# Kernel optimization log

Measured on AMD Instinct MI355X. Metric: run time of the kernel, lower is better.

The kernel has to match this reference:

```python
import jax, jax.numpy as jnp
from jax import lax
import numpy as np
import math

DIM = 96      # channels
HEADS = 3     # num_heads
WS = 8        # window size
SHIFT = 4     # window_size // 2 (depth is odd -> shifted)
TLC = 64      # tlc_kernel
H = 264
W = 264


def _grid_idxes(h, w, k1, k2):
    # Faithful replication of the torch grids() tiling index logic (static ints).
    num_row = (h - 1) // k1 + 1
    num_col = (w - 1) // k2 + 1
    step_j = k2 if num_col == 1 else math.ceil((w - k2) / (num_col - 1) - 1e-8)
    step_i = k1 if num_row == 1 else math.ceil((h - k1) / (num_row - 1) - 1e-8)
    idxes = []
    i = 0
    last_i = False
    while i < h and not last_i:
        j = 0
        if i + k1 >= h:
            i = h - k1
            last_i = True
        last_j = False
        while j < w and not last_j:
            if j + k2 >= w:
                j = w - k2
                last_j = True
            idxes.append((i, j))
            j = j + step_j
        i = i + step_i
    return idxes


def setup_inputs() -> dict:
    key = jax.random.key(0)
    ks = jax.random.split(key, 4)
    return {
        "x": jax.random.normal(ks[0], (1, DIM, H, W), jnp.float32),
        "temperature": jnp.ones((HEADS, 1, 1), jnp.float32),
        "qkv_w": jax.random.normal(ks[1], (3 * DIM, DIM), jnp.float32) * 0.05,
        "dw_w": jax.random.normal(ks[2], (3 * DIM, 1, 3, 3), jnp.float32) * 0.1,
        "proj_w": jax.random.normal(ks[3], (DIM, DIM), jnp.float32) * 0.05,
    }


def reference(x, temperature, qkv_w, dw_w, proj_w):
    b, c, h, w = x.shape
    # depth % 2 == 1 -> cyclic shift
    x = jnp.roll(x, (-SHIFT, -SHIFT), axis=(2, 3))
    # 1x1 pointwise conv (no bias)
    qkv = jnp.einsum('oc,bchw->bohw', qkv_w, x)
    # 3x3 depthwise conv, padding 1
    qkv = lax.conv_general_dilated(
        qkv, dw_w, window_strides=(1, 1), padding=[(1, 1), (1, 1)],
        feature_group_count=3 * c, dimension_numbers=('NCHW', 'OIHW', 'NCHW'))
    # --- TLC grids: overlapping tiles (eval path, b == 1) ---
    k1, k2 = min(h, TLC), min(w, TLC)
    idxes = _grid_idxes(h, w, k1, k2)
    parts = jnp.concatenate([qkv[:, :, i:i + k1, j:j + k2] for (i, j) in idxes], axis=0)  # [T,3c,k1,k2]
    T, C3, th, tw = parts.shape
    nh, nw = th // WS, tw // WS
    # window partition: b c (h b0) (w b1) -> (b h w) c b0 b1 -> flatten spatial
    win = parts.reshape(T, C3, nh, WS, nw, WS).transpose(0, 2, 4, 1, 3, 5)
    win = win.reshape(T * nh * nw, C3, WS * WS)  # [Bw, 3c, 64]
    q, k, v = jnp.split(win, 3, axis=1)  # each [Bw, c, 64]
    ch = c // HEADS
    q = q.reshape(-1, HEADS, ch, WS * WS)
    k = k.reshape(-1, HEADS, ch, WS * WS)
    v = v.reshape(-1, HEADS, ch, WS * WS)
    # L2 normalize along token dim (F.normalize eps=1e-12)
    q = q / jnp.maximum(jnp.linalg.norm(q, axis=-1, keepdims=True), 1e-12)
    k = k / jnp.maximum(jnp.linalg.norm(k, axis=-1, keepdims=True), 1e-12)
    # channel attention: [Bw, head, ch, ch]
    attn = jax.nn.relu(jnp.einsum('bhcn,bhdn->bhcd', q, k) * temperature)
    out = jnp.einsum('bhcd,bhdn->bhcn', attn, v)  # [Bw, head, ch, 64]
    out = out.reshape(-1, c, WS, WS)
    # window merge back to tiles
    out = out.reshape(T, nh, nw, c, WS, WS).transpose(0, 3, 1, 4, 2, 5).reshape(T, c, th, tw)
    # --- TLC grids_inverse: scatter-add overlapping tiles and average ---
    preds = jnp.zeros((b, c, h, w), x.dtype)
    cnt = np.zeros((h, w), np.float32)
    for t, (i, j) in enumerate(idxes):
        preds = preds.at[0, :, i:i + k1, j:j + k2].add(out[t])
        cnt[i:i + k1, j:j + k2] += 1.0
    preds = preds / jnp.asarray(cnt)
    # 1x1 output projection
    out = jnp.einsum('oc,bchw->bohw', proj_w, preds)
    # undo cyclic shift
    return jnp.roll(out, (SHIFT, SHIFT), axis=(2, 3))
```

## Files before the change

### kernel.cpp

```cpp
#include <hip/hip_runtime.h>
#include <hip/hip_bf16.h>

#define HW_ 69696
#define W_ 264
#define H_ 264

typedef short bf16x8 __attribute__((ext_vector_type(8)));
typedef float f32x4 __attribute__((ext_vector_type(4)));

static __device__ __forceinline__ unsigned short f2b(float f) {
  __hip_bfloat16 h = __float2bfloat16(f);
  return *reinterpret_cast<unsigned short*>(&h);
}
static __device__ __forceinline__ float b2f(unsigned short u) {
  __hip_bfloat16 h;
  *reinterpret_cast<unsigned short*>(&h) = u;
  return __bfloat162float(h);
}
static __device__ __forceinline__ float lo_f(unsigned int u) {
  union { unsigned int i; float f; } c; c.i = u << 16; return c.f;
}
static __device__ __forceinline__ float hi_f(unsigned int u) {
  union { unsigned int i; float f; } c; c.i = u & 0xffff0000u; return c.f;
}

__global__ __launch_bounds__(256, 5) void k_gemm(const float* __restrict__ x,
                                                 const float* __restrict__ w,
                                                 unsigned short* __restrict__ outb) {
  __shared__ __align__(16) unsigned short As[96 * 104];

  const int tid = threadIdx.x;
  const int wid = tid >> 6, lane = tid & 63;
  const int quad = lane >> 4, lo = lane & 15;
  const int px0 = blockIdx.x * 64;
  const int px = px0 + wid * 16 + lo;

  const int y = px / W_, xx = px - y * W_;
  int y2 = y + 4; if (y2 >= H_) y2 -= H_;
  int x2 = xx + 4; if (x2 >= W_) x2 -= W_;
  const float* xb = x + y2 * W_ + x2;

  bf16x8 bfv[3];
#pragma unroll
  for (int ks = 0; ks < 3; ++ks) {
    const float* xp = xb + (size_t)(ks * 32 + quad * 8) * HW_;
    float f[8];
#pragma unroll
    for (int i = 0; i < 8; ++i) f[i] = xp[(size_t)i * HW_];
    union { bf16x8 v; unsigned short s[8]; } u;
#pragma unroll
    for (int i = 0; i < 8; ++i) u.s[i] = f2b(f[i]);
    bfv[ks] = u.v;
  }

  for (int oc = 0; oc < 3; ++oc) {
    __syncthreads();
    const float* wp = w + oc * 96 * 96;
    for (int l = tid; l < 96 * 24; l += 256) {
      int o = l / 24, c4 = (l - (l / 24) * 24) * 4;
      float4 v = *(const float4*)&wp[o * 96 + c4];
      unsigned int p0 = (unsigned int)f2b(v.x) | ((unsigned int)f2b(v.y) << 16);
      unsigned int p1 = (unsigned int)f2b(v.z) | ((unsigned int)f2b(v.w) << 16);
      *(uint2*)&As[o * 104 + c4] = make_uint2(p0, p1);
    }
    __syncthreads();

    f32x4 acc[6];
#pragma unroll
    for (int mt = 0; mt < 6; ++mt) acc[mt] = {0.f, 0.f, 0.f, 0.f};
#pragma unroll
    for (int ks = 0; ks < 3; ++ks) {
      const int kb = ks * 32 + quad * 8;
#pragma unroll
      for (int mt = 0; mt < 6; ++mt) {
        bf16x8 a = *(const bf16x8*)&As[(mt * 16 + lo) * 104 + kb];
        acc[mt] = __builtin_amdgcn_mfma_f32_16x16x32_bf16(a, bfv[ks], acc[mt], 0, 0, 0);
      }
    }

#pragma unroll
    for (int mt = 0; mt < 6; ++mt) {
      const int u = oc * 12 + 2 * mt + (quad >> 1);
      unsigned int p0 = (unsigned int)f2b(acc[mt][0]) | ((unsigned int)f2b(acc[mt][1]) << 16);
      unsigned int p1 = (unsigned int)f2b(acc[mt][2]) | ((unsigned int)f2b(acc[mt][3]) << 16);
      *(uint2*)((char*)outb + ((size_t)u * HW_ + px) * 16 + (quad & 1) * 8) = make_uint2(p0, p1);
    }
  }
}

__global__ __launch_bounds__(256, 3) void k_dwattn(const unsigned short* __restrict__ qkvb,
                                                   const float* __restrict__ dwv,
                                                   const float* __restrict__ temp,
                                                   unsigned short* __restrict__ tout) {
  __shared__ __align__(16) unsigned short outS[64 * 296];
  __shared__ __align__(16) uint4 stg[4][100];
  __shared__ __align__(16) unsigned short attnL[3 * 32 * 40];
  __shared__ float invn[3 * 32];

  const int tid = threadIdx.x;
  const int bx = blockIdx.x;
  const int pair = ((bx & 7) << 2) | (bx >> 3);
  const int t = blockIdx.y;
  const int i0 = (t / 5) * 50, j0 = (t % 5) * 50;
  const int wy = pair >> 2, wx0 = (pair & 3) * 2;

  const int h = tid >> 6, lane = tid & 63;
  const int w_ = __builtin_amdgcn_readfirstlane(h);
  const int quad = lane >> 4, lo = lane & 15;

  uint4* stgW = &stg[w_][0];
  const int r0 = lane >> 3, c0 = lane & 7;
  const int sy0 = lane / 10, sx0 = lane - sy0 * 10;
  const int ii1 = lane + 64;
  const int sy1 = ii1 / 10, sx1 = ii1 - sy1 * 10;
  const uint4* qb4 = (const uint4*)qkvb;

  for (int w2 = 0; w2 < 2; ++w2) {
    const int wx = wx0 + w2;
    const int gy0 = i0 + wy * 8, gx0 = j0 + wx * 8;

    {
      const int gyA = gy0 - 1 + sy0, gxA = gx0 - 1 + sx0;
      const int gyB = gy0 - 1 + sy1, gxB = gx0 - 1 + sx1;
      const bool okA = (unsigned)gyA < (unsigned)H_ && (unsigned)gxA < (unsigned)W_;
      const bool okB = ii1 < 100 && (unsigned)gyB < (unsigned)H_ && (unsigned)gxB < (unsigned)W_;
      const size_t offA = (size_t)gyA * W_ + gxA;
      const size_t offB = (size_t)gyB * W_ + gxB;

      uint4 vA = okA ? qb4[(size_t)w_ * HW_ + offA] : make_uint4(0u, 0u, 0u, 0u);
      uint4 vB = okB ? qb4[(size_t)w_ * HW_ + offB] : make_uint4(0u, 0u, 0u, 0u);

      for (int k = 0; k < 9; ++k) {
        const int u = k * 4 + w_;
        stgW[lane] = vA;
        if (ii1 < 100) stgW[ii1] = vB;
        if (k < 8) {
          vA = okA ? qb4[(size_t)(u + 4) * HW_ + offA] : make_uint4(0u, 0u, 0u, 0u);
          vB = okB ? qb4[(size_t)(u + 4) * HW_ + offB] : make_uint4(0u, 0u, 0u, 0u);
        }
        asm volatile("s_waitcnt lgkmcnt(0)" ::: "memory");
        __builtin_amdgcn_sched_barrier(0);

        const float* wp = dwv + u * 72;
        float acc[8] = {0.f, 0.f, 0.f, 0.f, 0.f, 0.f, 0.f, 0.f};
#pragma unroll
        for (int dy = 0; dy < 3; ++dy)
#pragma unroll
          for (int dx = 0; dx < 3; ++dx) {
            uint4 v = stgW[(r0 + dy) * 10 + (c0 + dx)];
            float w0 = wp[0 * 9 + dy * 3 + dx], w1 = wp[1 * 9 + dy * 3 + dx];
            float w2v = wp[2 * 9 + dy * 3 + dx], w3 = wp[3 * 9 + dy * 3 + dx];
            float w4 = wp[4 * 9 + dy * 3 + dx], w5 = wp[5 * 9 + dy * 3 + dx];
            float w6 = wp[6 * 9 + dy * 3 + dx], w7 = wp[7 * 9 + dy * 3 + dx];
            acc[0] += w0 * lo_f(v.x); acc[1] += w1 * hi_f(v.x);
            acc[2] += w2v * lo_f(v.y); acc[3] += w3 * hi_f(v.y);
            acc[4] += w4 * lo_f(v.z); acc[5] += w5 * hi_f(v.z);
            acc[6] += w6 * lo_f(v.w); acc[7] += w7 * hi_f(v.w);
          }
        uint4 o;
        o.x = (unsigned int)f2b(acc[0]) | ((unsigned int)f2b(acc[1]) << 16);
        o.y = (unsigned int)f2b(acc[2]) | ((unsigned int)f2b(acc[3]) << 16);
        o.z = (unsigned int)f2b(acc[4]) | ((unsigned int)f2b(acc[5]) << 16);
        o.w = (unsigned int)f2b(acc[6]) | ((unsigned int)f2b(acc[7]) << 16);
        *(uint4*)&outS[lane * 296 + u * 8] = o;
      }
    }
    __syncthreads();

    const int cb = h * 32;
    f32x4 S[2][2];
    bf16x8 qf[2][2], kf[2][2];
    float ivk[2];
    if (h < 3) {
#pragma unroll
      for (int mt = 0; mt < 2; ++mt)
#pragma unroll
        for (int kt = 0; kt < 2; ++kt) {
          const int rr = kt * 4 + quad;
          const int cq = cb + mt * 16 + lo;
          const int ck = 96 + cq;
          bf16x8 q8, k8;
#pragma unroll
          for (int j = 0; j < 8; ++j) {
            q8[j] = (short)outS[(rr * 8 + j) * 296 + cq];
            k8[j] = (short)outS[(rr * 8 + j) * 296 + ck];
          }
          qf[mt][kt] = q8;
          kf[mt][kt] = k8;
        }

#pragma unroll
      for (int mt = 0; mt < 2; ++mt)
#pragma unroll
        for (int nt = 0; nt < 2; ++nt) {
          S[mt][nt] = {0.f, 0.f, 0.f, 0.f};
#pragma unroll
          for (int kt = 0; kt < 2; ++kt)
            S[mt][nt] = __builtin_amdgcn_mfma_f32_16x16x32_bf16(qf[mt][kt], kf[nt][kt], S[mt][nt], 0, 0, 0);
        }

#pragma unroll
      for (int mt = 0; mt < 2; ++mt) {
        float sq = 0.f, sk = 0.f;
#pragma unroll
        for (int kt = 0; kt < 2; ++kt)
#pragma unroll
          for (int j = 0; j < 8; ++j) {
            float a = b2f((unsigned short)qf[mt][kt][j]);
            float b = b2f((unsigned short)kf[mt][kt][j]);
            sq += a * a;
            sk += b * b;
          }
        sq += __shfl_xor(sq, 16);
        sq += __shfl_xor(sq, 32);
        sk += __shfl_xor(sk, 16);
        sk += __shfl_xor(sk, 32);
        if (quad == 0) invn[h * 32 + mt * 16 + lo] = 1.f / fmaxf(sqrtf(sq), 1e-12f);
        ivk[mt] = 1.f / fmaxf(sqrtf(sk), 1e-12f);
      }
    }
    __syncthreads();

    if (h < 3) {
      const float ts = temp[h];
#pragma unroll
      for (int mt = 0; mt < 2; ++mt)
#pragma unroll
        for (int nt = 0; nt < 2; ++nt)
#pragma unroll
          for (int r = 0; r < 4; ++r) {
            int c = mt * 16 + quad * 4 + r;
            float v = S[mt][nt][r] * invn[h * 32 + c] * ivk[nt] * ts;
            attnL[(h * 32 + c) * 40 + nt * 16 + lo] = f2b(fmaxf(v, 0.f));
          }
    }
    __syncthreads();

    f32x4 O[2][4];
    if (h < 3) {
      bf16x8 af[2];
#pragma unroll
      for (int mt = 0; mt < 2; ++mt)
        af[mt] = *(const bf16x8*)&attnL[(h * 32 + mt * 16 + lo) * 40 + quad * 8];

      const int uv = 24 + h * 4 + quad;
#pragma unroll
      for (int nt = 0; nt < 4; ++nt) {
        const int px = nt * 16 + lo;
        uint4 vraw = *(const uint4*)&outS[px * 296 + uv * 8];
        bf16x8 vf = *reinterpret_cast<bf16x8*>(&vraw);
#pragma unroll
        for (int mt = 0; mt < 2; ++mt) {
          f32x4 z = {0.f, 0.f, 0.f, 0.f};
          O[mt][nt] = __builtin_amdgcn_mfma_f32_16x16x32_bf16(af[mt], vf, z, 0, 0, 0);
        }
      }
    }
    __syncthreads();

    unsigned short* Cs = outS;
    if (h < 3) {
#pragma unroll
      for (int mt = 0; mt < 2; ++mt)
#pragma unroll
        for (int nt = 0; nt < 4; ++nt) {
          const int px = nt * 16 + lo;
          unsigned int p0 = (unsigned int)f2b(O[mt][nt][0]) | ((unsigned int)f2b(O[mt][nt][1]) << 16);
          unsigned int p1 = (unsigned int)f2b(O[mt][nt][2]) | ((unsigned int)f2b(O[mt][nt][3]) << 16);
          *(uint2*)&Cs[px * 104 + cb + mt * 16 + quad * 4] = make_uint2(p0, p1);
        }
    }
    __syncthreads();

    for (int idx = tid; idx < 64 * 12; idx += 256) {
      int u = idx >> 6, rec = idx & 63;
      int r = rec >> 3, j = rec & 7;
      size_t local = (size_t)(wy * 8 + r) * 64 + wx * 8 + j;
      ((uint4*)tout)[((size_t)t * 12 + u) * 4096 + local] = ((const uint4*)(Cs + rec * 104))[u];
    }
    __syncthreads();
  }
}

__global__ __launch_bounds__(256, 5) void k_avgproj(const float* __restrict__ w,
                                                    const unsigned short* __restrict__ tout,
                                                    float* __restrict__ outf) {
  __shared__ __align__(16) unsigned short As[96 * 104];
  const int tid = threadIdx.x;
  const int wid = tid >> 6, lane = tid & 63;
  const int quad = lane >> 4, lo = lane & 15;
  const int px0 = blockIdx.x * 64;
  const int px = px0 + wid * 16 + lo;

  for (int l = tid; l < 96 * 24; l += 256) {
    int o = l / 24, c4 = (l - (l / 24) * 24) * 4;
    float4 v = *(const float4*)&w[o * 96 + c4];
    unsigned int p0 = (unsigned int)f2b(v.x) | ((unsigned int)f2b(v.y) << 16);
    unsigned int p1 = (unsigned int)f2b(v.z) | ((unsigned int)f2b(v.w) << 16);
    *(uint2*)&As[o * 104 + c4] = make_uint2(p0, p1);
  }

  const int y = px / W_, xx = px - y * W_;
  int loy = (y >= 64) ? (y - 14) / 50 : 0;
  int hiy = y / 50; if (hiy > 4) hiy = 4;
  int lox = (xx >= 64) ? (xx - 14) / 50 : 0;
  int hix = xx / 50; if (hix > 4) hix = 4;
  float a24[24];
#pragma unroll
  for (int i = 0; i < 24; ++i) a24[i] = 0.f;
  int cnt = 0;
  for (int ty = loy; ty <= hiy; ++ty)
    for (int tx = lox; tx <= hix; ++tx) {
      size_t local = (size_t)((y - ty * 50) << 6) + (xx - tx * 50);
      const uint4* rp = (const uint4*)tout +
                        ((size_t)(ty * 5 + tx) * 12 + quad) * 4096 + local;
#pragma unroll
      for (int ks = 0; ks < 3; ++ks) {
        uint4 v = rp[(size_t)ks * 4 * 4096];
        a24[ks * 8 + 0] += lo_f(v.x); a24[ks * 8 + 1] += hi_f(v.x);
        a24[ks * 8 + 2] += lo_f(v.y); a24[ks * 8 + 3] += hi_f(v.y);
        a24[ks * 8 + 4] += lo_f(v.z); a24[ks * 8 + 5] += hi_f(v.z);
        a24[ks * 8 + 6] += lo_f(v.w); a24[ks * 8 + 7] += hi_f(v.w);
      }
      ++cnt;
    }
  const float inv = 1.f / (float)cnt;
  bf16x8 bfv[3];
#pragma unroll
  for (int ks = 0; ks < 3; ++ks) {
    union { bf16x8 v; unsigned short s[8]; } u;
#pragma unroll
    for (int i = 0; i < 8; ++i) u.s[i] = f2b(a24[ks * 8 + i] * inv);
    bfv[ks] = u.v;
  }
  __syncthreads();

  f32x4 acc[6];
#pragma unroll
  for (int mt = 0; mt < 6; ++mt) acc[mt] = {0.f, 0.f, 0.f, 0.f};
#pragma unroll
  for (int ks = 0; ks < 3; ++ks) {
    const int kb = ks * 32 + quad * 8;
#pragma unroll
    for (int mt = 0; mt < 6; ++mt) {
      bf16x8 a = *(const bf16x8*)&As[(mt * 16 + lo) * 104 + kb];
      acc[mt] = __builtin_amdgcn_mfma_f32_16x16x32_bf16(a, bfv[ks], acc[mt], 0, 0, 0);
    }
  }

  {
    int y2 = y + 4; if (y2 >= H_) y2 -= H_;
    int x2 = xx + 4; if (x2 >= W_) x2 -= W_;
    int tp = y2 * W_ + x2;
#pragma unroll
    for (int mt = 0; mt < 6; ++mt) {
      int row = mt * 16 + quad * 4;
#pragma unroll
      for (int r = 0; r < 4; ++r)
        outf[(size_t)(row + r) * HW_ + tp] = acc[mt][r];
    }
  }
}

extern "C" void kernel_launch(void* const* d_in, const int* in_sizes, int n_in,
                              void* d_out, int out_size, void* d_ws, size_t ws_size,
                              hipStream_t stream) {
  (void)in_sizes; (void)n_in; (void)out_size; (void)ws_size;
  const float* x = (const float*)d_in[0];
  const float* temp = (const float*)d_in[1];
  const float* qkvw = (const float*)d_in[2];
  const float* dww = (const float*)d_in[3];
  const float* projw = (const float*)d_in[4];
  float* out = (float*)d_out;

  char* ws = (char*)d_ws;
  const size_t SZQ = (size_t)288 * HW_ * 2;
  unsigned short* qkvb = (unsigned short*)ws;
  unsigned short* tout = (unsigned short*)(ws + SZQ);

  k_gemm<<<dim3(1089), 256, 0, stream>>>(x, qkvw, qkvb);
  k_dwattn<<<dim3(32, 25), 256, 0, stream>>>(qkvb, dww, temp, tout);
  k_avgproj<<<dim3(1089), 256, 0, stream>>>(projw, tout, out);
}
```

Baseline: 150.2 us.

## Process one window per block with channel-major Q/K smem and batched loads

The depthwise+attention kernel now handles one 8x8 window per block instead of two, doubling the grid. All nine staged global loads are issued up front into registers, so they no longer trickle in one per iteration. Q/K are written channel-major into a separate shared buffer so that MFMA operands become single 16-byte reads instead of eight scalar gathers, and V gets its own compact buffer. The exchange is higher register pressure from holding 18 uint4s, with occupancy still capped by launch bounds of 3, plus twice as many blocks.

```diff
diff --git a/kernel.cpp b/kernel.cpp
--- a/kernel.cpp
+++ b/kernel.cpp
@@ -92,193 +92,189 @@
                                                    const float* __restrict__ dwv,
                                                    const float* __restrict__ temp,
                                                    unsigned short* __restrict__ tout) {
-  __shared__ __align__(16) unsigned short outS[64 * 296];
-  __shared__ __align__(16) uint4 stg[4][100];
-  __shared__ __align__(16) unsigned short attnL[3 * 32 * 40];
-  __shared__ float invn[3 * 32];
+  __shared__ __align__(16) char smem[49024];
+  unsigned short* qkS = (unsigned short*)smem;
+  unsigned short* vS = (unsigned short*)(smem + 27648);
+  uint4* stgBase = (uint4*)(smem + 40960);
+  unsigned short* attnL = (unsigned short*)(smem + 40960);
+  float* invn = (float*)(smem + 48640);
+  unsigned short* Cs = (unsigned short*)smem;
 
   const int tid = threadIdx.x;
-  const int bx = blockIdx.x;
-  const int pair = ((bx & 7) << 2) | (bx >> 3);
+  const int wi = ((blockIdx.x & 7) << 3) | (blockIdx.x >> 3);
   const int t = blockIdx.y;
   const int i0 = (t / 5) * 50, j0 = (t % 5) * 50;
-  const int wy = pair >> 2, wx0 = (pair & 3) * 2;
+  const int wy = wi >> 3, wx = wi & 7;
+  const int gy0 = i0 + wy * 8, gx0 = j0 + wx * 8;
 
   const int h = tid >> 6, lane = tid & 63;
   const int w_ = __builtin_amdgcn_readfirstlane(h);
   const int quad = lane >> 4, lo = lane & 15;
 
-  uint4* stgW = &stg[w_][0];
-  const int r0 = lane >> 3, c0 = lane & 7;
-  const int sy0 = lane / 10, sx0 = lane - sy0 * 10;
-  const int ii1 = lane + 64;
-  const int sy1 = ii1 / 10, sx1 = ii1 - sy1 * 10;
-  const uint4* qb4 = (const uint4*)qkvb;
-
-  for (int w2 = 0; w2 < 2; ++w2) {
-    const int wx = wx0 + w2;
-    const int gy0 = i0 + wy * 8, gx0 = j0 + wx * 8;
-
-    {
-      const int gyA = gy0 - 1 + sy0, gxA = gx0 - 1 + sx0;
-      const int gyB = gy0 - 1 + sy1, gxB = gx0 - 1 + sx1;
-      const bool okA = (unsigned)gyA < (unsigned)H_ && (unsigned)gxA < (unsigned)W_;
-      const bool okB = ii1 < 100 && (unsigned)gyB < (unsigned)H_ && (unsigned)gxB < (unsigned)W_;
-      const size_t offA = (size_t)gyA * W_ + gxA;
-      const size_t offB = (size_t)gyB * W_ + gxB;
-
-      uint4 vA = okA ? qb4[(size_t)w_ * HW_ + offA] : make_uint4(0u, 0u, 0u, 0u);
-      uint4 vB = okB ? qb4[(size_t)w_ * HW_ + offB] : make_uint4(0u, 0u, 0u, 0u);
-
-      for (int k = 0; k < 9; ++k) {
-        const int u = k * 4 + w_;
-        stgW[lane] = vA;
-        if (ii1 < 100) stgW[ii1] = vB;
-        if (k < 8) {
-          vA = okA ? qb4[(size_t)(u + 4) * HW_ + offA] : make_uint4(0u, 0u, 0u, 0u);
-          vB = okB ? qb4[(size_t)(u + 4) * HW_ + offB] : make_uint4(0u, 0u, 0u, 0u);
+  {
+    uint4* stgW = stgBase + w_ * 100;
+    const int r0 = lane >> 3, c0 = lane & 7;
+    const int sy0 = lane / 10, sx0 = lane - sy0 * 10;
+    const int ii1 = lane + 64;
+    const int sy1 = ii1 / 10, sx1 = ii1 - sy1 * 10;
+    const int gyA = gy0 - 1 + sy0, gxA = gx0 - 1 + sx0;
+    const int gyB = gy0 - 1 + sy1, gxB = gx0 - 1 + sx1;
+    const bool okA = (unsigned)gyA < (unsigned)H_ && (unsigned)gxA < (unsigned)W_;
+    const bool okB = ii1 < 100 && (unsigned)gyB < (unsigned)H_ && (unsigned)gxB < (unsigned)W_;
+    const size_t offA = (size_t)gyA * W_ + gxA;
+    const size_t offB = (size_t)gyB * W_ + gxB;
+    const uint4* qb4 = (const uint4*)qkvb;
+
+    uint4 vA[9], vB[9];
+#pragma unroll
+    for (int k = 0; k < 9; ++k) {
+      const int u = k * 4 + w_;
+      vA[k] = okA ? qb4[(size_t)u * HW_ + offA] : make_uint4(0u, 0u, 0u, 0u);
+      vB[k] = okB ? qb4[(size_t)u * HW_ + offB] : make_uint4(0u, 0u, 0u, 0u);
+    }
+
+#pragma unroll
+    for (int k = 0; k < 9; ++k) {
+      const int u = k * 4 + w_;
+      stgW[lane] = vA[k];
+      if (ii1 < 100) stgW[ii1] = vB[k];
+      asm volatile("s_waitcnt lgkmcnt(0)" ::: "memory");
+      __builtin_amdgcn_sched_barrier(0);
+
+      const float* wp = dwv + u * 72;
+      float acc[8] = {0.f, 0.f, 0.f, 0.f, 0.f, 0.f, 0.f, 0.f};
+#pragma unroll
+      for (int dy = 0; dy < 3; ++dy)
+#pragma unroll
+        for (int dx = 0; dx < 3; ++dx) {
+          uint4 v = stgW[(r0 + dy) * 10 + (c0 + dx)];
+          float w0 = wp[0 * 9 + dy * 3 + dx], w1 = wp[1 * 9 + dy * 3 + dx];
+          float w2 = wp[2 * 9 + dy * 3 + dx], w3 = wp[3 * 9 + dy * 3 + dx];
+          float w4 = wp[4 * 9 + dy * 3 + dx], w5 = wp[5 * 9 + dy * 3 + dx];
+          float w6 = wp[6 * 9 + dy * 3 + dx], w7 = wp[7 * 9 + dy * 3 + dx];
+          acc[0] += w0 * lo_f(v.x); acc[1] += w1 * hi_f(v.x);
+          acc[2] += w2 * lo_f(v.y); acc[3] += w3 * hi_f(v.y);
+          acc[4] += w4 * lo_f(v.z); acc[5] += w5 * hi_f(v.z);
+          acc[6] += w6 * lo_f(v.w); acc[7] += w7 * hi_f(v.w);
         }
-        asm volatile("s_waitcnt lgkmcnt(0)" ::: "memory");
-        __builtin_amdgcn_sched_barrier(0);
-
-        const float* wp = dwv + u * 72;
-        float acc[8] = {0.f, 0.f, 0.f, 0.f, 0.f, 0.f, 0.f, 0.f};
-#pragma unroll
-        for (int dy = 0; dy < 3; ++dy)
-#pragma unroll
-          for (int dx = 0; dx < 3; ++dx) {
-            uint4 v = stgW[(r0 + dy) * 10 + (c0 + dx)];
-            float w0 = wp[0 * 9 + dy * 3 + dx], w1 = wp[1 * 9 + dy * 3 + dx];
-            float w2v = wp[2 * 9 + dy * 3 + dx], w3 = wp[3 * 9 + dy * 3 + dx];
-            float w4 = wp[4 * 9 + dy * 3 + dx], w5 = wp[5 * 9 + dy * 3 + dx];
-            float w6 = wp[6 * 9 + dy * 3 + dx], w7 = wp[7 * 9 + dy * 3 + dx];
-            acc[0] += w0 * lo_f(v.x); acc[1] += w1 * hi_f(v.x);
-            acc[2] += w2v * lo_f(v.y); acc[3] += w3 * hi_f(v.y);
-            acc[4] += w4 * lo_f(v.z); acc[5] += w5 * hi_f(v.z);
-            acc[6] += w6 * lo_f(v.w); acc[7] += w7 * hi_f(v.w);
-          }
+      if (k < 6) {
+#pragma unroll
+        for (int i = 0; i < 8; ++i)
+          qkS[(u * 8 + i) * 72 + lane] = f2b(acc[i]);
+      } else {
         uint4 o;
         o.x = (unsigned int)f2b(acc[0]) | ((unsigned int)f2b(acc[1]) << 16);
         o.y = (unsigned int)f2b(acc[2]) | ((unsigned int)f2b(acc[3]) << 16);
         o.z = (unsigned int)f2b(acc[4]) | ((unsigned int)f2b(acc[5]) << 16);
         o.w = (unsigned int)f2b(acc[6]) | ((unsigned int)f2b(acc[7]) << 16);
-        *(uint4*)&outS[lane * 296 + u * 8] = o;
-      }
-    }
-    __syncthreads();
-
-    const int cb = h * 32;
-    f32x4 S[2][2];
-    bf16x8 qf[2][2], kf[2][2];
-    float ivk[2];
-    if (h < 3) {
-#pragma unroll
-      for (int mt = 0; mt < 2; ++mt)
-#pragma unroll
-        for (int kt = 0; kt < 2; ++kt) {
-          const int rr = kt * 4 + quad;
-          const int cq = cb + mt * 16 + lo;
-          const int ck = 96 + cq;
-          bf16x8 q8, k8;
-#pragma unroll
-          for (int j = 0; j < 8; ++j) {
-            q8[j] = (short)outS[(rr * 8 + j) * 296 + cq];
-            k8[j] = (short)outS[(rr * 8 + j) * 296 + ck];
-          }
-          qf[mt][kt] = q8;
-          kf[mt][kt] = k8;
+        *(uint4*)&vS[lane * 104 + (u - 24) * 8] = o;
+      }
+    }
+  }
+  __syncthreads();
+
+  const int cb = h * 32;
+  f32x4 S[2][2];
+  bf16x8 qf[2][2], kf[2][2];
+  float ivk[2];
+  if (h < 3) {
+#pragma unroll
+    for (int mt = 0; mt < 2; ++mt)
+#pragma unroll
+      for (int kt = 0; kt < 2; ++kt) {
+        const int row = cb + mt * 16 + lo;
+        const int pxc = (kt * 4 + quad) * 8;
+        qf[mt][kt] = *(const bf16x8*)&qkS[row * 72 + pxc];
+        kf[mt][kt] = *(const bf16x8*)&qkS[(96 + row) * 72 + pxc];
+      }
+
+#pragma unroll
+    for (int mt = 0; mt < 2; ++mt)
+#pragma unroll
+      for (int nt = 0; nt < 2; ++nt) {
+        S[mt][nt] = {0.f, 0.f, 0.f, 0.f};
+#pragma unroll
+        for (int kt = 0; kt < 2; ++kt)
+          S[mt][nt] = __builtin_amdgcn_mfma_f32_16x16x32_bf16(qf[mt][kt], kf[nt][kt], S[mt][nt], 0, 0, 0);
+      }
+
+#pragma unroll
+    for (int mt = 0; mt < 2; ++mt) {
+      float sq = 0.f, sk = 0.f;
+#pragma unroll
+      for (int kt = 0; kt < 2; ++kt)
+#pragma unroll
+        for (int j = 0; j < 8; ++j) {
+          float a = b2f((unsigned short)qf[mt][kt][j]);
+          float b = b2f((unsigned short)kf[mt][kt][j]);
+          sq += a * a;
+          sk += b * b;
         }
-
-#pragma unroll
-      for (int mt = 0; mt < 2; ++mt)
-#pragma unroll
-        for (int nt = 0; nt < 2; ++nt) {
-          S[mt][nt] = {0.f, 0.f, 0.f, 0.f};
-#pragma unroll
-          for (int kt = 0; kt < 2; ++kt)
-            S[mt][nt] = __builtin_amdgcn_mfma_f32_16x16x32_bf16(qf[mt][kt], kf[nt][kt], S[mt][nt], 0, 0, 0);
+      sq += __shfl_xor(sq, 16);
+      sq += __shfl_xor(sq, 32);
+      sk += __shfl_xor(sk, 16);
+      sk += __shfl_xor(sk, 32);
+      if (quad == 0) invn[h * 32 + mt * 16 + lo] = 1.f / fmaxf(sqrtf(sq), 1e-12f);
+      ivk[mt] = 1.f / fmaxf(sqrtf(sk), 1e-12f);
+    }
+  }
+  __syncthreads();
+
+  if (h < 3) {
+    const float ts = temp[h];
+#pragma unroll
+    for (int mt = 0; mt < 2; ++mt)
+#pragma unroll
+      for (int nt = 0; nt < 2; ++nt)
+#pragma unroll
+        for (int r = 0; r < 4; ++r) {
+          int c = mt * 16 + quad * 4 + r;
+          float v = S[mt][nt][r] * invn[h * 32 + c] * ivk[nt] * ts;
+          attnL[(h * 32 + c) * 40 + nt * 16 + lo] = f2b(fmaxf(v, 0.f));
         }
-
+  }
+  __syncthreads();
+
+  f32x4 O[2][4];
+  if (h < 3) {
+    bf16x8 af[2];
+#pragma unroll
+    for (int mt = 0; mt < 2; ++mt)
+      af[mt] = *(const bf16x8*)&attnL[(h * 32 + mt * 16 + lo) * 40 + quad * 8];
+
+    const int uv = h * 4 + quad;
+#pragma unroll
+    for (int nt = 0; nt < 4; ++nt) {
+      const int px = nt * 16 + lo;
+      uint4 vraw = *(const uint4*)&vS[px * 104 + uv * 8];
+      bf16x8 vf = *reinterpret_cast<bf16x8*>(&vraw);
 #pragma unroll
       for (int mt = 0; mt < 2; ++mt) {
-        float sq = 0.f, sk = 0.f;
-#pragma unroll
-        for (int kt = 0; kt < 2; ++kt)
-#pragma unroll
-          for (int j = 0; j < 8; ++j) {
-            float a = b2f((unsigned short)qf[mt][kt][j]);
-            float b = b2f((unsigned short)kf[mt][kt][j]);
-            sq += a * a;
-            sk += b * b;
-          }
-        sq += __shfl_xor(sq, 16);
-        sq += __shfl_xor(sq, 32);
-        sk += __shfl_xor(sk, 16);
-        sk += __shfl_xor(sk, 32);
-        if (quad == 0) invn[h * 32 + mt * 16 + lo] = 1.f / fmaxf(sqrtf(sq), 1e-12f);
-        ivk[mt] = 1.f / fmaxf(sqrtf(sk), 1e-12f);
-      }
-    }
-    __syncthreads();
-
-    if (h < 3) {
-      const float ts = temp[h];
-#pragma unroll
-      for (int mt = 0; mt < 2; ++mt)
-#pragma unroll
-        for (int nt = 0; nt < 2; ++nt)
-#pragma unroll
-          for (int r = 0; r < 4; ++r) {
-            int c = mt * 16 + quad * 4 + r;
-            float v = S[mt][nt][r] * invn[h * 32 + c] * ivk[nt] * ts;
-            attnL[(h * 32 + c) * 40 + nt * 16 + lo] = f2b(fmaxf(v, 0.f));
-          }
-    }
-    __syncthreads();
-
-    f32x4 O[2][4];
-    if (h < 3) {
-      bf16x8 af[2];
-#pragma unroll
-      for (int mt = 0; mt < 2; ++mt)
-        af[mt] = *(const bf16x8*)&attnL[(h * 32 + mt * 16 + lo) * 40 + quad * 8];
-
-      const int uv = 24 + h * 4 + quad;
+        f32x4 z = {0.f, 0.f, 0.f, 0.f};
+        O[mt][nt] = __builtin_amdgcn_mfma_f32_16x16x32_bf16(af[mt], vf, z, 0, 0, 0);
+      }
+    }
+  }
+  __syncthreads();
+
+  if (h < 3) {
+#pragma unroll
+    for (int mt = 0; mt < 2; ++mt)
 #pragma unroll
       for (int nt = 0; nt < 4; ++nt) {
         const int px = nt * 16 + lo;
-        uint4 vraw = *(const uint4*)&outS[px * 296 + uv * 8];
-        bf16x8 vf = *reinterpret_cast<bf16x8*>(&vraw);
-#pragma unroll
-        for (int mt = 0; mt < 2; ++mt) {
-          f32x4 z = {0.f, 0.f, 0.f, 0.f};
-          O[mt][nt] = __builtin_amdgcn_mfma_f32_16x16x32_bf16(af[mt], vf, z, 0, 0, 0);
-        }
-      }
-    }
-    __syncthreads();
-
-    unsigned short* Cs = outS;
-    if (h < 3) {
-#pragma unroll
-      for (int mt = 0; mt < 2; ++mt)
-#pragma unroll
-        for (int nt = 0; nt < 4; ++nt) {
-          const int px = nt * 16 + lo;
-          unsigned int p0 = (unsigned int)f2b(O[mt][nt][0]) | ((unsigned int)f2b(O[mt][nt][1]) << 16);
-          unsigned int p1 = (unsigned int)f2b(O[mt][nt][2]) | ((unsigned int)f2b(O[mt][nt][3]) << 16);
-          *(uint2*)&Cs[px * 104 + cb + mt * 16 + quad * 4] = make_uint2(p0, p1);
-        }
-    }
-    __syncthreads();
-
-    for (int idx = tid; idx < 64 * 12; idx += 256) {
-      int u = idx >> 6, rec = idx & 63;
-      int r = rec >> 3, j = rec & 7;
-      size_t local = (size_t)(wy * 8 + r) * 64 + wx * 8 + j;
-      ((uint4*)tout)[((size_t)t * 12 + u) * 4096 + local] = ((const uint4*)(Cs + rec * 104))[u];
-    }
-    __syncthreads();
+        unsigned int p0 = (unsigned int)f2b(O[mt][nt][0]) | ((unsigned int)f2b(O[mt][nt][1]) << 16);
+        unsigned int p1 = (unsigned int)f2b(O[mt][nt][2]) | ((unsigned int)f2b(O[mt][nt][3]) << 16);
+        *(uint2*)&Cs[px * 104 + cb + mt * 16 + quad * 4] = make_uint2(p0, p1);
+      }
+  }
+  __syncthreads();
+
+  for (int idx = tid; idx < 64 * 12; idx += 256) {
+    int u = idx >> 6, rec = idx & 63;
+    int r = rec >> 3, j = rec & 7;
+    size_t local = (size_t)(wy * 8 + r) * 64 + wx * 8 + j;
+    ((uint4*)tout)[((size_t)t * 12 + u) * 4096 + local] = ((const uint4*)(Cs + rec * 104))[u];
   }
 }
 
@@ -379,6 +375,6 @@
   unsigned short* tout = (unsigned short*)(ws + SZQ);
 
   k_gemm<<<dim3(1089), 256, 0, stream>>>(x, qkvw, qkvb);
-  k_dwattn<<<dim3(32, 25), 256, 0, stream>>>(qkvb, dww, temp, tout);
+  k_dwattn<<<dim3(64, 25), 256, 0, stream>>>(qkvb, dww, temp, tout);
   k_avgproj<<<dim3(1089), 256, 0, stream>>>(projw, tout, out);
 }
```

Result: faster. 147.0 us (-2.1%).
